# Performance work log

Measured on AMD Instinct MI355X. Metric: run time of the kernel, lower is better.

Reference implementation:

```python
import jax, jax.numpy as jnp
import numpy as np
import math

EMBED_DIM = 512
NUM_CLASSES = 100000
BATCH = 512
MARGIN = 0.5
SCALE = 64.0
EASY_MARGIN = False
COS_M = math.cos(MARGIN)
SIN_M = math.sin(MARGIN)
TH = math.cos(math.pi - MARGIN)
MM = math.sin(math.pi - MARGIN) * MARGIN


def setup_inputs() -> dict:
    key = jax.random.key(0)
    k1, k2, k3 = jax.random.split(key, 3)
    inp = jax.random.normal(k1, (BATCH, EMBED_DIM), dtype=jnp.float32)
    # xavier-uniform init for weight [num_classes, embedding_dim]
    limit = math.sqrt(6.0 / (NUM_CLASSES + EMBED_DIM))
    weight = jax.random.uniform(k2, (NUM_CLASSES, EMBED_DIM), dtype=jnp.float32,
                                minval=-limit, maxval=limit)
    target = jax.random.randint(k3, (BATCH,), 0, NUM_CLASSES, dtype=jnp.int64)
    return {"input": inp, "weight": weight, "target": target}


def _l2_normalize(x, axis, eps=1e-12):
    # matches F.normalize(p=2): x / max(||x||, eps)
    n = jnp.sqrt(jnp.sum(x * x, axis=axis, keepdims=True))
    return x / jnp.maximum(n, eps)


def reference(input, weight, target):
    x = _l2_normalize(input, axis=1)                      # [B, D]
    w = _l2_normalize(weight, axis=1)                     # [C, D]
    cosine = jnp.einsum('bd,cd->bc', x, w)                # [B, C]
    # margin only affects the target logit; compute it per-row (same math as
    # the full-matrix where + one_hot blend in the original).
    cos_t = jnp.take_along_axis(cosine, target[:, None].astype(jnp.int32), axis=1)[:, 0]  # [B]
    sin_t = jnp.sqrt(jnp.clip(1.0 - cos_t * cos_t, 0.0, None))
    phi_t = cos_t * COS_M - sin_t * SIN_M
    if EASY_MARGIN:
        phi_t = jnp.where(cos_t > 0, phi_t, cos_t)
    else:
        phi_t = jnp.where(cos_t > TH, phi_t, cos_t - MM)
    # cross-entropy with scaled logits: logsumexp over modified logits - target logit
    # modified logits differ from `cosine*SCALE` only at the target column.
    rows = jnp.arange(cosine.shape[0])
    logits = cosine.at[rows, target.astype(jnp.int32)].set(phi_t) * SCALE  # [B, C]
    lse = jax.scipy.special.logsumexp(logits, axis=1)     # [B]
    loss = jnp.mean(lse - SCALE * phi_t)
    return loss
```

## Files before the change

kernel.cpp:

```cpp
#include <hip/hip_runtime.h>
#include <math.h>


#define NB 512
#define ND 512
#define NC 100000
#define BK 32
#define NCHUNK 16
#define CT 64
#define FSCALE 64.0f
#define C_COS_M 0.8775825618903728f
#define C_SIN_M 0.479425538604203f
#define C_TH  (-0.8775825618903728f)
#define C_MM  0.2397127693021015f

typedef __bf16 bf16x8 __attribute__((ext_vector_type(8)));
typedef __bf16 bf16x4 __attribute__((ext_vector_type(4)));
typedef float  f32x4  __attribute__((ext_vector_type(4)));
typedef __attribute__((address_space(1))) unsigned int GU;
typedef __attribute__((address_space(3))) unsigned int LU;

__global__ void pack_x_kernel(const float* __restrict__ x, __bf16* __restrict__ xp) {
  const int b = blockIdx.x;
  const int t = threadIdx.x;
  float4 v = reinterpret_cast<const float4*>(x + (size_t)b * ND)[t];
  float ss = v.x*v.x + v.y*v.y + v.z*v.z + v.w*v.w;
  #pragma unroll
  for (int m = 1; m < 64; m <<= 1) ss += __shfl_xor(ss, m);
  __shared__ float sred[2];
  if ((t & 63) == 0) sred[t >> 6] = ss;
  __syncthreads();
  const float rn = rsqrtf(fmaxf(sred[0] + sred[1], 1e-24f));
  bf16x4 o;
  o[0] = (__bf16)(v.x * rn); o[1] = (__bf16)(v.y * rn);
  o[2] = (__bf16)(v.z * rn); o[3] = (__bf16)(v.w * rn);
  const int k = 4 * t;
  __bf16* dst = xp + ((size_t)(k >> 5) * NB + b) * BK + (k & 31);
  *reinterpret_cast<bf16x4*>(dst) = o;
}

__global__ void cosphi_kernel(const float* __restrict__ x, const float* __restrict__ w,
                              const int* __restrict__ tgt,
                              float* __restrict__ cos_t, float* __restrict__ phi_t) {
  const int b = blockIdx.x;
  const int lane = threadIdx.x;
  const int t = tgt[b];
  const float4* xr = reinterpret_cast<const float4*>(x + (size_t)b * ND);
  const float4* wr = reinterpret_cast<const float4*>(w + (size_t)t * ND);
  float dp = 0.f, xs = 0.f, ws = 0.f;
  #pragma unroll
  for (int j = 0; j < 2; ++j) {
    float4 xv = xr[lane * 2 + j];
    float4 wv = wr[lane * 2 + j];
    dp += xv.x*wv.x + xv.y*wv.y + xv.z*wv.z + xv.w*wv.w;
    xs += xv.x*xv.x + xv.y*xv.y + xv.z*xv.z + xv.w*xv.w;
    ws += wv.x*wv.x + wv.y*wv.y + wv.z*wv.z + wv.w*wv.w;
  }
  #pragma unroll
  for (int m = 1; m < 64; m <<= 1) {
    dp += __shfl_xor(dp, m);
    xs += __shfl_xor(xs, m);
    ws += __shfl_xor(ws, m);
  }
  if (lane == 0) {
    float c = dp * rsqrtf(fmaxf(xs, 1e-24f)) * rsqrtf(fmaxf(ws, 1e-24f));
    c = fminf(fmaxf(c, -1.f), 1.f);
    float s = sqrtf(fmaxf(1.f - c * c, 0.f));
    float phi = c * C_COS_M - s * C_SIN_M;
    phi = (c > C_TH) ? phi : (c - C_MM);
    cos_t[b] = c;
    phi_t[b] = phi;
  }
}

__global__ __launch_bounds__(512) void gemm_lse_kernel(
    const __bf16* __restrict__ xp, const float* __restrict__ w,
    float* __restrict__ gsum) {
  __shared__ __align__(16) __bf16 As[NB * BK];
  __shared__ __align__(16) __bf16 Bs[CT * BK];
  __shared__ float wss[CT];

  const int tid  = threadIdx.x;
  const int wv   = tid >> 6;
  const int lane = tid & 63;
  const int bc   = blockIdx.x * CT;

  const int wr = tid >> 3;
  const int wp = tid & 7;
  const long long wrow = (long long)min(bc + wr, NC - 1);
  const float4* wsrc = reinterpret_cast<const float4*>(w + wrow * (long long)ND);

  float wsq = 0.f;
  f32x4 acc[4][4] = {};

  const int m_w = wv * 64;
  const int qa  = (lane >> 4) * 8;
  const int ra  = lane & 15;

  for (int i = 0; i < NCHUNK; ++i) {
    __syncthreads();
    {
      const char* g = reinterpret_cast<const char*>(xp)
                      + (size_t)i * (NB * BK * 2) + wv * 1024 + lane * 16;
      char* l = reinterpret_cast<char*>(As) + wv * 1024;
      #pragma unroll
      for (int j = 0; j < 4; ++j) {
        __builtin_amdgcn_global_load_lds((GU*)(g + j * 8192), (LU*)(l + j * 8192),
                                         16, 0, 0);
      }
    }
    {
      float4 v = wsrc[i * 8 + wp];
      wsq += v.x*v.x + v.y*v.y + v.z*v.z + v.w*v.w;
      bf16x4 pk;
      pk[0] = (__bf16)v.x; pk[1] = (__bf16)v.y;
      pk[2] = (__bf16)v.z; pk[3] = (__bf16)v.w;
      *reinterpret_cast<bf16x4*>(Bs + wr * BK + wp * 4) = pk;
    }
    __syncthreads();

    bf16x8 af[4], bfr[4];
    #pragma unroll
    for (int rt = 0; rt < 4; ++rt)
      af[rt] = *reinterpret_cast<const bf16x8*>(As + (m_w + rt * 16 + ra) * BK + qa);
    #pragma unroll
    for (int ct = 0; ct < 4; ++ct)
      bfr[ct] = *reinterpret_cast<const bf16x8*>(Bs + (ct * 16 + ra) * BK + qa);
    #pragma unroll
    for (int rt = 0; rt < 4; ++rt)
      #pragma unroll
      for (int ct = 0; ct < 4; ++ct)
        acc[rt][ct] = __builtin_amdgcn_mfma_f32_16x16x32_bf16(af[rt], bfr[ct],
                                                              acc[rt][ct], 0, 0, 0);
  }

  wsq += __shfl_xor(wsq, 1);
  wsq += __shfl_xor(wsq, 2);
  wsq += __shfl_xor(wsq, 4);
  if (wp == 0) wss[wr] = wsq;
  __syncthreads();

  const int col_l = lane & 15;
  const int quad  = lane >> 4;
  float rnw[4];
  int   vmask[4];
  #pragma unroll
  for (int ct = 0; ct < 4; ++ct) {
    rnw[ct]   = rsqrtf(fmaxf(wss[ct * 16 + col_l], 1e-24f));
    vmask[ct] = (bc + ct * 16 + col_l) < NC;
  }
  #pragma unroll
  for (int rt = 0; rt < 4; ++rt) {
    #pragma unroll
    for (int r = 0; r < 4; ++r) {
      float es = 0.f;
      #pragma unroll
      for (int ct = 0; ct < 4; ++ct) {
        float cosv = acc[rt][ct][r] * rnw[ct];
        float e = __expf(fmaf(FSCALE, cosv, -FSCALE));
        es += vmask[ct] ? e : 0.f;
      }
      es += __shfl_xor(es, 1);
      es += __shfl_xor(es, 2);
      es += __shfl_xor(es, 4);
      es += __shfl_xor(es, 8);
      if (col_l == 0) {
        atomicAdd(&gsum[m_w + rt * 16 + quad * 4 + r], es);
      }
    }
  }
}

__global__ void finalize_kernel(const float* __restrict__ gsum,
                                const float* __restrict__ cos_t,
                                const float* __restrict__ phi_t,
                                float* __restrict__ out) {
  const int b = threadIdx.x;
  const float c = cos_t[b];
  const float p = phi_t[b];
  float corr = gsum[b] - __expf(fmaf(FSCALE, c, -FSCALE))
                       + __expf(fmaf(FSCALE, p, -FSCALE));
  corr = fmaxf(corr, 1e-38f);
  float lb = FSCALE + logf(corr) - FSCALE * p;
  #pragma unroll
  for (int m = 1; m < 64; m <<= 1) lb += __shfl_xor(lb, m);
  __shared__ float pr[8];
  if ((b & 63) == 0) pr[b >> 6] = lb;
  __syncthreads();
  if (b == 0) {
    float tot = 0.f;
    #pragma unroll
    for (int j = 0; j < 8; ++j) tot += pr[j];
    out[0] = tot * (1.0f / NB);
  }
}

extern "C" void kernel_launch(void* const* d_in, const int* in_sizes, int n_in,
                              void* d_out, int out_size, void* d_ws, size_t ws_size,
                              hipStream_t stream) {
  const float* x  = (const float*)d_in[0];
  const float* w  = (const float*)d_in[1];
  const int* tgt  = (const int*)d_in[2];
  float* out      = (float*)d_out;

  __bf16* xp   = (__bf16*)d_ws;
  float* gsum  = (float*)((char*)d_ws + (size_t)NB * ND * 2);
  float* cos_t = gsum + NB;
  float* phi_t = cos_t + NB;

  hipMemsetAsync(gsum, 0, NB * sizeof(float), stream);
  pack_x_kernel<<<NB, 128, 0, stream>>>(x, xp);
  cosphi_kernel<<<NB, 64, 0, stream>>>(x, w, tgt, cos_t, phi_t);
  const int nblk = (NC + CT - 1) / CT;
  gemm_lse_kernel<<<nblk, 512, 0, stream>>>(xp, w, gsum);
  finalize_kernel<<<1, 512, 0, stream>>>(gsum, cos_t, phi_t, out);
}
```

Baseline: 428.9 us.

## Pre-normalize weights to swizzled bf16 and split GEMM over batch halves

```diff
diff --git a/kernel.cpp b/kernel.cpp
--- a/kernel.cpp
+++ b/kernel.cpp
@@ -8,6 +8,8 @@
 #define BK 32
 #define NCHUNK 16
 #define CT 64
+#define MT 256
+#define NCT 1563
 #define FSCALE 64.0f
 #define C_COS_M 0.8775825618903728f
 #define C_SIN_M 0.479425538604203f
@@ -19,6 +21,7 @@
 typedef float  f32x4  __attribute__((ext_vector_type(4)));
 typedef __attribute__((address_space(1))) unsigned int GU;
 typedef __attribute__((address_space(3))) unsigned int LU;
+
 
 __global__ void pack_x_kernel(const float* __restrict__ x, __bf16* __restrict__ xp) {
   const int b = blockIdx.x;
@@ -34,14 +37,52 @@
   bf16x4 o;
   o[0] = (__bf16)(v.x * rn); o[1] = (__bf16)(v.y * rn);
   o[2] = (__bf16)(v.z * rn); o[3] = (__bf16)(v.w * rn);
-  const int k = 4 * t;
-  __bf16* dst = xp + ((size_t)(k >> 5) * NB + b) * BK + (k & 31);
+  const int mh = b >> 8, r = b & 255;
+  const int i  = t >> 3;
+  const int g  = (t >> 1) & 3;
+  const int gp = g ^ ((r >> 1) & 3);
+  __bf16* dst = xp + ((size_t)(mh * NCHUNK + i) * MT + r) * BK + gp * 8 + (t & 1) * 4;
   *reinterpret_cast<bf16x4*>(dst) = o;
+}
+
+__global__ __launch_bounds__(256) void prep_w_kernel(const float* __restrict__ w,
+                                                     __bf16* __restrict__ wp) {
+  const int b    = blockIdx.x;
+  const int wv   = threadIdx.x >> 6;
+  const int lane = threadIdx.x & 63;
+  const int i = lane >> 2;
+  const int g = lane & 3;
+  for (int it = 0; it < 8; ++it) {
+    #pragma unroll
+    for (int h = 0; h < 2; ++h) {
+      const int r = wv * 16 + h * 8 + it;
+      const int c = b * CT + r;
+      float4 v0 = {0.f,0.f,0.f,0.f}, v1 = {0.f,0.f,0.f,0.f};
+      if (c < NC) {
+        const float4* src = reinterpret_cast<const float4*>(w + (size_t)c * ND) + lane * 2;
+        v0 = src[0]; v1 = src[1];
+      }
+      float ss = v0.x*v0.x + v0.y*v0.y + v0.z*v0.z + v0.w*v0.w
+               + v1.x*v1.x + v1.y*v1.y + v1.z*v1.z + v1.w*v1.w;
+      #pragma unroll
+      for (int m = 1; m < 64; m <<= 1) ss += __shfl_xor(ss, m);
+      const float rn = rsqrtf(fmaxf(ss, 1e-24f));
+      bf16x8 o;
+      o[0] = (__bf16)(v0.x * rn); o[1] = (__bf16)(v0.y * rn);
+      o[2] = (__bf16)(v0.z * rn); o[3] = (__bf16)(v0.w * rn);
+      o[4] = (__bf16)(v1.x * rn); o[5] = (__bf16)(v1.y * rn);
+      o[6] = (__bf16)(v1.z * rn); o[7] = (__bf16)(v1.w * rn);
+      const int gp = g ^ ((r >> 1) & 3);
+      __bf16* dst = wp + ((size_t)(b * NCHUNK + i) * CT + r) * BK + gp * 8;
+      *reinterpret_cast<bf16x8*>(dst) = o;
+    }
+  }
 }
 
 __global__ void cosphi_kernel(const float* __restrict__ x, const float* __restrict__ w,
                               const int* __restrict__ tgt,
-                              float* __restrict__ cos_t, float* __restrict__ phi_t) {
+                              float* __restrict__ cos_t, float* __restrict__ phi_t,
+                              float* __restrict__ gsum) {
   const int b = blockIdx.x;
   const int lane = threadIdx.x;
   const int t = tgt[b];
@@ -70,103 +111,75 @@
     phi = (c > C_TH) ? phi : (c - C_MM);
     cos_t[b] = c;
     phi_t[b] = phi;
-  }
-}
-
-__global__ __launch_bounds__(512) void gemm_lse_kernel(
-    const __bf16* __restrict__ xp, const float* __restrict__ w,
+    gsum[b] = 0.f;
+  }
+}
+
+__global__ __launch_bounds__(256, 4) void gemm_lse_kernel(
+    const __bf16* __restrict__ xp, const __bf16* __restrict__ wp,
     float* __restrict__ gsum) {
-  __shared__ __align__(16) __bf16 As[NB * BK];
+  __shared__ __align__(16) __bf16 As[MT * BK];
   __shared__ __align__(16) __bf16 Bs[CT * BK];
-  __shared__ float wss[CT];
 
   const int tid  = threadIdx.x;
   const int wv   = tid >> 6;
   const int lane = tid & 63;
-  const int bc   = blockIdx.x * CT;
-
-  const int wr = tid >> 3;
-  const int wp = tid & 7;
-  const long long wrow = (long long)min(bc + wr, NC - 1);
-  const float4* wsrc = reinterpret_cast<const float4*>(w + wrow * (long long)ND);
-
-  float wsq = 0.f;
+  const int ct   = blockIdx.x >> 1;
+  const int mh   = blockIdx.x & 1;
+
+  const int ra  = lane & 15;
+  const int q   = lane >> 4;
+  const int gp  = q ^ ((ra >> 1) & 3);
+
+  const char* abase = reinterpret_cast<const char*>(xp) + (size_t)mh * (NCHUNK * MT * BK * 2);
+  const char* bbase = reinterpret_cast<const char*>(wp) + (size_t)ct * (NCHUNK * CT * BK * 2);
+
   f32x4 acc[4][4] = {};
-
-  const int m_w = wv * 64;
-  const int qa  = (lane >> 4) * 8;
-  const int ra  = lane & 15;
 
   for (int i = 0; i < NCHUNK; ++i) {
     __syncthreads();
     {
-      const char* g = reinterpret_cast<const char*>(xp)
-                      + (size_t)i * (NB * BK * 2) + wv * 1024 + lane * 16;
-      char* l = reinterpret_cast<char*>(As) + wv * 1024;
-      #pragma unroll
-      for (int j = 0; j < 4; ++j) {
-        __builtin_amdgcn_global_load_lds((GU*)(g + j * 8192), (LU*)(l + j * 8192),
+      const char* ga = abase + i * (MT * BK * 2) + wv * 4096 + lane * 16;
+      char* la = reinterpret_cast<char*>(As) + wv * 4096;
+      #pragma unroll
+      for (int j = 0; j < 4; ++j)
+        __builtin_amdgcn_global_load_lds((const GU*)(ga + j * 1024), (LU*)(la + j * 1024),
                                          16, 0, 0);
-      }
     }
     {
-      float4 v = wsrc[i * 8 + wp];
-      wsq += v.x*v.x + v.y*v.y + v.z*v.z + v.w*v.w;
-      bf16x4 pk;
-      pk[0] = (__bf16)v.x; pk[1] = (__bf16)v.y;
-      pk[2] = (__bf16)v.z; pk[3] = (__bf16)v.w;
-      *reinterpret_cast<bf16x4*>(Bs + wr * BK + wp * 4) = pk;
+      const char* gb = bbase + i * (CT * BK * 2) + wv * 1024 + lane * 16;
+      char* lb = reinterpret_cast<char*>(Bs) + wv * 1024;
+      __builtin_amdgcn_global_load_lds((const GU*)gb, (LU*)lb, 16, 0, 0);
     }
     __syncthreads();
 
-    bf16x8 af[4], bfr[4];
+    bf16x8 af[4];
     #pragma unroll
     for (int rt = 0; rt < 4; ++rt)
-      af[rt] = *reinterpret_cast<const bf16x8*>(As + (m_w + rt * 16 + ra) * BK + qa);
-    #pragma unroll
-    for (int ct = 0; ct < 4; ++ct)
-      bfr[ct] = *reinterpret_cast<const bf16x8*>(Bs + (ct * 16 + ra) * BK + qa);
-    #pragma unroll
-    for (int rt = 0; rt < 4; ++rt)
-      #pragma unroll
-      for (int ct = 0; ct < 4; ++ct)
-        acc[rt][ct] = __builtin_amdgcn_mfma_f32_16x16x32_bf16(af[rt], bfr[ct],
-                                                              acc[rt][ct], 0, 0, 0);
-  }
-
-  wsq += __shfl_xor(wsq, 1);
-  wsq += __shfl_xor(wsq, 2);
-  wsq += __shfl_xor(wsq, 4);
-  if (wp == 0) wss[wr] = wsq;
-  __syncthreads();
-
-  const int col_l = lane & 15;
-  const int quad  = lane >> 4;
-  float rnw[4];
-  int   vmask[4];
-  #pragma unroll
-  for (int ct = 0; ct < 4; ++ct) {
-    rnw[ct]   = rsqrtf(fmaxf(wss[ct * 16 + col_l], 1e-24f));
-    vmask[ct] = (bc + ct * 16 + col_l) < NC;
-  }
+      af[rt] = *reinterpret_cast<const bf16x8*>(As + (wv * 64 + rt * 16 + ra) * BK + gp * 8);
+    #pragma unroll
+    for (int c4 = 0; c4 < 4; ++c4) {
+      bf16x8 bfr = *reinterpret_cast<const bf16x8*>(Bs + (c4 * 16 + ra) * BK + gp * 8);
+      #pragma unroll
+      for (int rt = 0; rt < 4; ++rt)
+        acc[rt][c4] = __builtin_amdgcn_mfma_f32_16x16x32_bf16(af[rt], bfr, acc[rt][c4], 0, 0, 0);
+    }
+  }
+
   #pragma unroll
   for (int rt = 0; rt < 4; ++rt) {
     #pragma unroll
     for (int r = 0; r < 4; ++r) {
       float es = 0.f;
       #pragma unroll
-      for (int ct = 0; ct < 4; ++ct) {
-        float cosv = acc[rt][ct][r] * rnw[ct];
-        float e = __expf(fmaf(FSCALE, cosv, -FSCALE));
-        es += vmask[ct] ? e : 0.f;
-      }
+      for (int c4 = 0; c4 < 4; ++c4)
+        es += __expf(fmaf(FSCALE, acc[rt][c4][r], -FSCALE));
       es += __shfl_xor(es, 1);
       es += __shfl_xor(es, 2);
       es += __shfl_xor(es, 4);
       es += __shfl_xor(es, 8);
-      if (col_l == 0) {
-        atomicAdd(&gsum[m_w + rt * 16 + quad * 4 + r], es);
-      }
+      if (ra == 0)
+        atomicAdd(&gsum[mh * MT + wv * 64 + rt * 16 + q * 4 + r], es);
     }
   }
 }
@@ -203,15 +216,17 @@
   const int* tgt  = (const int*)d_in[2];
   float* out      = (float*)d_out;
 
+  const size_t XP_BYTES = (size_t)2 * NCHUNK * MT * BK * 2;
+  const size_t WP_BYTES = (size_t)NCT * NCHUNK * CT * BK * 2;
   __bf16* xp   = (__bf16*)d_ws;
-  float* gsum  = (float*)((char*)d_ws + (size_t)NB * ND * 2);
+  __bf16* wp   = (__bf16*)((char*)d_ws + XP_BYTES);
+  float* gsum  = (float*)((char*)d_ws + XP_BYTES + WP_BYTES);
   float* cos_t = gsum + NB;
   float* phi_t = cos_t + NB;
 
-  hipMemsetAsync(gsum, 0, NB * sizeof(float), stream);
   pack_x_kernel<<<NB, 128, 0, stream>>>(x, xp);
-  cosphi_kernel<<<NB, 64, 0, stream>>>(x, w, tgt, cos_t, phi_t);
-  const int nblk = (NC + CT - 1) / CT;
-  gemm_lse_kernel<<<nblk, 512, 0, stream>>>(xp, w, gsum);
+  prep_w_kernel<<<NCT, 256, 0, stream>>>(w, wp);
+  cosphi_kernel<<<NB, 64, 0, stream>>>(x, w, tgt, cos_t, phi_t, gsum);
+  gemm_lse_kernel<<<NCT * 2, 256, 0, stream>>>(xp, wp, gsum);
   finalize_kernel<<<1, 512, 0, stream>>>(gsum, cos_t, phi_t, out);
 }
```

New measurement: 531.2 us. 23.8% more time.

## Double GEMM column tile, swizzle LDS layout, prefetch weight chunks into registers

Applied to the files above, without the earlier changes.

```diff
diff --git a/kernel.cpp b/kernel.cpp
--- a/kernel.cpp
+++ b/kernel.cpp
@@ -7,7 +7,8 @@
 #define NC 100000
 #define BK 32
 #define NCHUNK 16
-#define CT 64
+#define CT 128
+#define NT 782
 #define FSCALE 64.0f
 #define C_COS_M 0.8775825618903728f
 #define C_SIN_M 0.479425538604203f
@@ -19,6 +20,7 @@
 typedef float  f32x4  __attribute__((ext_vector_type(4)));
 typedef __attribute__((address_space(1))) unsigned int GU;
 typedef __attribute__((address_space(3))) unsigned int LU;
+
 
 __global__ void pack_x_kernel(const float* __restrict__ x, __bf16* __restrict__ xp) {
   const int b = blockIdx.x;
@@ -34,14 +36,17 @@
   bf16x4 o;
   o[0] = (__bf16)(v.x * rn); o[1] = (__bf16)(v.y * rn);
   o[2] = (__bf16)(v.z * rn); o[3] = (__bf16)(v.w * rn);
-  const int k = 4 * t;
-  __bf16* dst = xp + ((size_t)(k >> 5) * NB + b) * BK + (k & 31);
+  const int i  = t >> 3;
+  const int g  = (t >> 1) & 3;
+  const int gp = g ^ ((b >> 1) & 3);
+  __bf16* dst = xp + ((size_t)i * NB + b) * BK + gp * 8 + (t & 1) * 4;
   *reinterpret_cast<bf16x4*>(dst) = o;
 }
 
 __global__ void cosphi_kernel(const float* __restrict__ x, const float* __restrict__ w,
                               const int* __restrict__ tgt,
-                              float* __restrict__ cos_t, float* __restrict__ phi_t) {
+                              float* __restrict__ cos_t, float* __restrict__ phi_t,
+                              float* __restrict__ gsum) {
   const int b = blockIdx.x;
   const int lane = threadIdx.x;
   const int t = tgt[b];
@@ -70,10 +75,11 @@
     phi = (c > C_TH) ? phi : (c - C_MM);
     cos_t[b] = c;
     phi_t[b] = phi;
-  }
-}
-
-__global__ __launch_bounds__(512) void gemm_lse_kernel(
+    gsum[b] = 0.f;
+  }
+}
+
+__global__ __launch_bounds__(512, 2) void gemm_lse_kernel(
     const __bf16* __restrict__ xp, const float* __restrict__ w,
     float* __restrict__ gsum) {
   __shared__ __align__(16) __bf16 As[NB * BK];
@@ -83,90 +89,87 @@
   const int tid  = threadIdx.x;
   const int wv   = tid >> 6;
   const int lane = tid & 63;
-  const int bc   = blockIdx.x * CT;
-
-  const int wr = tid >> 3;
-  const int wp = tid & 7;
-  const long long wrow = (long long)min(bc + wr, NC - 1);
-  const float4* wsrc = reinterpret_cast<const float4*>(w + wrow * (long long)ND);
+  const int nt   = blockIdx.x;
+
+  const int ra = lane & 15;
+  const int q  = lane >> 4;
+  const int gp = q ^ ((ra >> 1) & 3);
+
+  const int wr = tid >> 2;
+  const int wq = tid & 3;
+  const long long brow = (long long)nt * CT + wr;
+  const bool valid = brow < NC;
+  const float* wsrc = w + (valid ? brow : 0) * (long long)ND + wq * 8;
+  const int bgp = wq ^ ((wr >> 1) & 3);
+
+  const float4 z4 = {0.f, 0.f, 0.f, 0.f};
+  float4 p0 = valid ? *reinterpret_cast<const float4*>(wsrc)     : z4;
+  float4 p1 = valid ? *reinterpret_cast<const float4*>(wsrc + 4) : z4;
 
   float wsq = 0.f;
-  f32x4 acc[4][4] = {};
-
-  const int m_w = wv * 64;
-  const int qa  = (lane >> 4) * 8;
-  const int ra  = lane & 15;
-
+  f32x4 acc[4][8] = {};
+
+  #pragma unroll
   for (int i = 0; i < NCHUNK; ++i) {
     __syncthreads();
     {
-      const char* g = reinterpret_cast<const char*>(xp)
-                      + (size_t)i * (NB * BK * 2) + wv * 1024 + lane * 16;
-      char* l = reinterpret_cast<char*>(As) + wv * 1024;
+      const char* ga = reinterpret_cast<const char*>(xp)
+                       + (size_t)i * (NB * BK * 2) + wv * 4096 + lane * 16;
+      char* la = reinterpret_cast<char*>(As) + wv * 4096;
       #pragma unroll
-      for (int j = 0; j < 4; ++j) {
-        __builtin_amdgcn_global_load_lds((GU*)(g + j * 8192), (LU*)(l + j * 8192),
-                                         16, 0, 0);
-      }
-    }
+      for (int j = 0; j < 4; ++j)
+        __builtin_amdgcn_global_load_lds((const GU*)(ga + j * 1024),
+                                         (LU*)(la + j * 1024), 16, 0, 0);
+    }
+    wsq += p0.x*p0.x + p0.y*p0.y + p0.z*p0.z + p0.w*p0.w
+         + p1.x*p1.x + p1.y*p1.y + p1.z*p1.z + p1.w*p1.w;
     {
-      float4 v = wsrc[i * 8 + wp];
-      wsq += v.x*v.x + v.y*v.y + v.z*v.z + v.w*v.w;
-      bf16x4 pk;
-      pk[0] = (__bf16)v.x; pk[1] = (__bf16)v.y;
-      pk[2] = (__bf16)v.z; pk[3] = (__bf16)v.w;
-      *reinterpret_cast<bf16x4*>(Bs + wr * BK + wp * 4) = pk;
+      bf16x8 ob;
+      ob[0] = (__bf16)p0.x; ob[1] = (__bf16)p0.y; ob[2] = (__bf16)p0.z; ob[3] = (__bf16)p0.w;
+      ob[4] = (__bf16)p1.x; ob[5] = (__bf16)p1.y; ob[6] = (__bf16)p1.z; ob[7] = (__bf16)p1.w;
+      *reinterpret_cast<bf16x8*>(Bs + wr * BK + bgp * 8) = ob;
     }
     __syncthreads();
-
-    bf16x8 af[4], bfr[4];
+    if (i < NCHUNK - 1) {
+      p0 = valid ? *reinterpret_cast<const float4*>(wsrc + (i + 1) * BK)     : z4;
+      p1 = valid ? *reinterpret_cast<const float4*>(wsrc + (i + 1) * BK + 4) : z4;
+    }
+    bf16x8 af[4];
     #pragma unroll
     for (int rt = 0; rt < 4; ++rt)
-      af[rt] = *reinterpret_cast<const bf16x8*>(As + (m_w + rt * 16 + ra) * BK + qa);
-    #pragma unroll
-    for (int ct = 0; ct < 4; ++ct)
-      bfr[ct] = *reinterpret_cast<const bf16x8*>(Bs + (ct * 16 + ra) * BK + qa);
-    #pragma unroll
-    for (int rt = 0; rt < 4; ++rt)
+      af[rt] = *reinterpret_cast<const bf16x8*>(As + (wv * 64 + rt * 16 + ra) * BK + gp * 8);
+    #pragma unroll
+    for (int ct = 0; ct < 8; ++ct) {
+      bf16x8 bfr = *reinterpret_cast<const bf16x8*>(Bs + (ct * 16 + ra) * BK + gp * 8);
       #pragma unroll
-      for (int ct = 0; ct < 4; ++ct)
-        acc[rt][ct] = __builtin_amdgcn_mfma_f32_16x16x32_bf16(af[rt], bfr[ct],
-                                                              acc[rt][ct], 0, 0, 0);
+      for (int rt = 0; rt < 4; ++rt)
+        acc[rt][ct] = __builtin_amdgcn_mfma_f32_16x16x32_bf16(af[rt], bfr, acc[rt][ct], 0, 0, 0);
+    }
   }
 
   wsq += __shfl_xor(wsq, 1);
   wsq += __shfl_xor(wsq, 2);
-  wsq += __shfl_xor(wsq, 4);
-  if (wp == 0) wss[wr] = wsq;
+  if (wq == 0) wss[wr] = wsq;
   __syncthreads();
 
-  const int col_l = lane & 15;
-  const int quad  = lane >> 4;
-  float rnw[4];
-  int   vmask[4];
-  #pragma unroll
-  for (int ct = 0; ct < 4; ++ct) {
-    rnw[ct]   = rsqrtf(fmaxf(wss[ct * 16 + col_l], 1e-24f));
-    vmask[ct] = (bc + ct * 16 + col_l) < NC;
-  }
+  float rnw[8];
+  #pragma unroll
+  for (int ct = 0; ct < 8; ++ct)
+    rnw[ct] = rsqrtf(fmaxf(wss[ct * 16 + ra], 1e-24f));
   #pragma unroll
   for (int rt = 0; rt < 4; ++rt) {
     #pragma unroll
     for (int r = 0; r < 4; ++r) {
       float es = 0.f;
       #pragma unroll
-      for (int ct = 0; ct < 4; ++ct) {
-        float cosv = acc[rt][ct][r] * rnw[ct];
-        float e = __expf(fmaf(FSCALE, cosv, -FSCALE));
-        es += vmask[ct] ? e : 0.f;
-      }
+      for (int ct = 0; ct < 8; ++ct)
+        es += __expf(fmaf(FSCALE, acc[rt][ct][r] * rnw[ct], -FSCALE));
       es += __shfl_xor(es, 1);
       es += __shfl_xor(es, 2);
       es += __shfl_xor(es, 4);
       es += __shfl_xor(es, 8);
-      if (col_l == 0) {
-        atomicAdd(&gsum[m_w + rt * 16 + quad * 4 + r], es);
-      }
+      if (ra == 0)
+        atomicAdd(&gsum[wv * 64 + rt * 16 + q * 4 + r], es);
     }
   }
 }
@@ -203,15 +206,14 @@
   const int* tgt  = (const int*)d_in[2];
   float* out      = (float*)d_out;
 
+  const size_t XP_BYTES = (size_t)NB * ND * 2;
   __bf16* xp   = (__bf16*)d_ws;
-  float* gsum  = (float*)((char*)d_ws + (size_t)NB * ND * 2);
+  float* gsum  = (float*)((char*)d_ws + XP_BYTES);
   float* cos_t = gsum + NB;
   float* phi_t = cos_t + NB;
 
-  hipMemsetAsync(gsum, 0, NB * sizeof(float), stream);
   pack_x_kernel<<<NB, 128, 0, stream>>>(x, xp);
-  cosphi_kernel<<<NB, 64, 0, stream>>>(x, w, tgt, cos_t, phi_t);
-  const int nblk = (NC + CT - 1) / CT;
-  gemm_lse_kernel<<<nblk, 512, 0, stream>>>(xp, w, gsum);
+  cosphi_kernel<<<NB, 64, 0, stream>>>(x, w, tgt, cos_t, phi_t, gsum);
+  gemm_lse_kernel<<<NT, 512, 0, stream>>>(xp, w, gsum);
   finalize_kernel<<<1, 512, 0, stream>>>(gsum, cos_t, phi_t, out);
 }
```

New measurement: 594.0 us. 1.38x slower.
